# Optimization experiments

Hardware: AMD Instinct MI355X
Metric: run time of the kernel (lower is better)

The kernel has to match this reference:

```python
import jax, jax.numpy as jnp
import numpy as np


def setup_inputs() -> dict:
    key = jax.random.key(0)
    k1, k2 = jax.random.split(key)
    T, H, E = 16384, 4096, 64
    hidden_states = jax.random.normal(k1, (T, H), dtype=jnp.float32)
    W = jax.random.normal(k2, (E, H), dtype=jnp.float32) * 0.02  # init std=0.02
    b = jnp.zeros((E,), dtype=jnp.float32)
    return {"hidden_states": hidden_states, "W": W, "b": b}


def reference(hidden_states, W, b):
    TOPK = 8
    # Linear: [T, H] @ [H, E] + [E] -> [T, E]
    router_logits = jnp.einsum("th,eh->te", hidden_states, W) + b
    router_probs = jax.nn.sigmoid(router_logits)
    routing_weights, routing_indices = jax.lax.top_k(router_probs, TOPK)
    routing_weights = routing_weights / jnp.sum(routing_weights, axis=-1, keepdims=True)
    return routing_weights, routing_indices, router_probs
```

## Files before the change

kernel.cpp:

```cpp
#include <hip/hip_runtime.h>
#include <math.h>

#define H 4096
#define E 64
#define TOPK 8
#define BM 64
#define BK 64
#define NKSTEP (BK / 32)
#define NTILE (H / BK)
#define TAU 1e-4f


typedef __attribute__((ext_vector_type(8))) short bf16x8;
typedef __attribute__((ext_vector_type(4))) float f32x4;

__device__ __forceinline__ unsigned short bf16_rne(float x) {
    unsigned int u = __float_as_uint(x);
    u += 0x7FFFu + ((u >> 16) & 1u);
    return (unsigned short)(u >> 16);
}
__device__ __forceinline__ float bf16_f32(unsigned short h) {
    return __uint_as_float(((unsigned int)h) << 16);
}

#define SPLIT2(F0, F1, HI, LO)                                          \
    {                                                                   \
        const unsigned short h0 = bf16_rne(F0), h1 = bf16_rne(F1);      \
        const unsigned short l0 = bf16_rne((F0) - bf16_f32(h0));        \
        const unsigned short l1 = bf16_rne((F1) - bf16_f32(h1));        \
        HI = (unsigned int)h0 | ((unsigned int)h1 << 16);               \
        LO = (unsigned int)l0 | ((unsigned int)l1 << 16);               \
    }

__global__ __launch_bounds__(256) void w_split(
    const float* __restrict__ W, unsigned short* __restrict__ Whi,
    unsigned short* __restrict__ Wlo)
{
    const size_t t = (size_t)blockIdx.x * 256 + threadIdx.x;
    const float4 v = *(const float4*)(W + t * 4);
    uint2 h, l;
    SPLIT2(v.x, v.y, h.x, l.x);
    SPLIT2(v.z, v.w, h.y, l.y);
    *(uint2*)(Whi + t * 4) = h;
    *(uint2*)(Wlo + t * 4) = l;
}

__global__ __launch_bounds__(512, 2) void router_gemm_topk(
    const float* __restrict__ A, const unsigned short* __restrict__ Whi,
    const unsigned short* __restrict__ Wlo, const float* __restrict__ bias,
    float* __restrict__ weights, float* __restrict__ indices,
    float* __restrict__ probs,
    int* __restrict__ flagcnt, int* __restrict__ flaglist, int cap)
{
    __shared__ unsigned short Ahi[BM][BK];
    __shared__ unsigned short Alo[BM][BK];
    __shared__ unsigned short Bhi[E][BK];
    __shared__ unsigned short Blo[E][BK];
    __shared__ float Llds[BM][E + 1];

    const int tid = threadIdx.x;
    const long row0 = (long)blockIdx.x * BM;

    const int srow = tid >> 3;
    const int sseg = tid & 7;
    const int slot = (sseg ^ (srow & 7)) * 8;

    const float* __restrict__ ap          = A   + (row0 + srow) * H + sseg * 8;
    const unsigned short* __restrict__ wh = Whi + (size_t)srow * H + sseg * 8;
    const unsigned short* __restrict__ wl = Wlo + (size_t)srow * H + sseg * 8;

    const int wv    = tid >> 6;
    const int l     = tid & 63;
    const int rbase = (wv & 3) * 16;
    const int cbase = (wv >> 2) * 32;
    const int lrow  = l & 15;
    const int khalf = l >> 4;

    f32x4 acc0 = {0.f, 0.f, 0.f, 0.f};
    f32x4 acc1 = {0.f, 0.f, 0.f, 0.f};

    float4 pa0 = *(const float4*)(ap + 0);
    float4 pa1 = *(const float4*)(ap + 4);
    uint4  pbh = *(const uint4*)(wh);
    uint4  pbl = *(const uint4*)(wl);

    for (int t = 0; t < NTILE; ++t) {
        uint4 h, lo;
        SPLIT2(pa0.x, pa0.y, h.x, lo.x);
        SPLIT2(pa0.z, pa0.w, h.y, lo.y);
        SPLIT2(pa1.x, pa1.y, h.z, lo.z);
        SPLIT2(pa1.z, pa1.w, h.w, lo.w);
        *(uint4*)(&Ahi[srow][slot]) = h;
        *(uint4*)(&Alo[srow][slot]) = lo;
        *(uint4*)(&Bhi[srow][slot]) = pbh;
        *(uint4*)(&Blo[srow][slot]) = pbl;
        __syncthreads();

        if (t + 1 < NTILE) {
            const int kn = (t + 1) * BK;
            pa0 = *(const float4*)(ap + kn + 0);
            pa1 = *(const float4*)(ap + kn + 4);
            pbh = *(const uint4*)(wh + kn);
            pbl = *(const uint4*)(wl + kn);
        }

#pragma unroll
        for (int s = 0; s < NKSTEP; ++s) {
            const int fs = ((s * 4 + khalf) ^ (lrow & 7)) * 8;
            const bf16x8 fah  = *(const bf16x8*)(&Ahi[rbase + lrow][fs]);
            const bf16x8 fal  = *(const bf16x8*)(&Alo[rbase + lrow][fs]);
            const bf16x8 fbh0 = *(const bf16x8*)(&Bhi[cbase + lrow][fs]);
            const bf16x8 fbl0 = *(const bf16x8*)(&Blo[cbase + lrow][fs]);
            const bf16x8 fbh1 = *(const bf16x8*)(&Bhi[cbase + 16 + lrow][fs]);
            const bf16x8 fbl1 = *(const bf16x8*)(&Blo[cbase + 16 + lrow][fs]);
            acc0 = __builtin_amdgcn_mfma_f32_16x16x32_bf16(fah, fbh0, acc0, 0, 0, 0);
            acc0 = __builtin_amdgcn_mfma_f32_16x16x32_bf16(fah, fbl0, acc0, 0, 0, 0);
            acc0 = __builtin_amdgcn_mfma_f32_16x16x32_bf16(fal, fbh0, acc0, 0, 0, 0);
            acc0 = __builtin_amdgcn_mfma_f32_16x16x32_bf16(fal, fbl0, acc0, 0, 0, 0);
            acc1 = __builtin_amdgcn_mfma_f32_16x16x32_bf16(fah, fbh1, acc1, 0, 0, 0);
            acc1 = __builtin_amdgcn_mfma_f32_16x16x32_bf16(fah, fbl1, acc1, 0, 0, 0);
            acc1 = __builtin_amdgcn_mfma_f32_16x16x32_bf16(fal, fbh1, acc1, 0, 0, 0);
            acc1 = __builtin_amdgcn_mfma_f32_16x16x32_bf16(fal, fbl1, acc1, 0, 0, 0);
        }
        __syncthreads();
    }

    {
        const int c0 = cbase + lrow;
        const int c1 = cbase + 16 + lrow;
        const float b0 = bias[c0], b1 = bias[c1];
#pragma unroll
        for (int r = 0; r < 4; ++r) {
            const int row = rbase + khalf * 4 + r;
            Llds[row][c0] = acc0[r] + b0;
            Llds[row][c1] = acc1[r] + b1;
        }
    }
    __syncthreads();

    {
        const int row = tid >> 3;
        const int c   = (tid & 7) * 8;
        float4 o0, o1;
        o0.x = 1.0f / (1.0f + __expf(-Llds[row][c + 0]));
        o0.y = 1.0f / (1.0f + __expf(-Llds[row][c + 1]));
        o0.z = 1.0f / (1.0f + __expf(-Llds[row][c + 2]));
        o0.w = 1.0f / (1.0f + __expf(-Llds[row][c + 3]));
        o1.x = 1.0f / (1.0f + __expf(-Llds[row][c + 4]));
        o1.y = 1.0f / (1.0f + __expf(-Llds[row][c + 5]));
        o1.z = 1.0f / (1.0f + __expf(-Llds[row][c + 6]));
        o1.w = 1.0f / (1.0f + __expf(-Llds[row][c + 7]));
        *(float4*)(probs + (row0 + row) * E + c + 0) = o0;
        *(float4*)(probs + (row0 + row) * E + c + 4) = o1;
    }

    if (tid < BM) {
        const int r = tid;
        unsigned long long taken = 0ull;
        float sv[TOPK + 1];
        int   si[TOPK + 1];
#pragma unroll
        for (int it = 0; it <= TOPK; ++it) {
            float best = -3.0e38f;
            int   bi   = 0;
            for (int j = 0; j < E; ++j) {
                if (!((taken >> j) & 1ull)) {
                    const float v = Llds[r][j];
                    if (v > best) { best = v; bi = j; }
                }
            }
            taken |= 1ull << bi;
            sv[it] = best;
            si[it] = bi;
        }
        float w8[TOPK];
        float sum = 0.0f;
#pragma unroll
        for (int it = 0; it < TOPK; ++it) {
            w8[it] = 1.0f / (1.0f + __expf(-sv[it]));
            sum += w8[it];
        }
        const float inv = 1.0f / sum;
#pragma unroll
        for (int it = 0; it < TOPK; ++it) {
            weights[(row0 + r) * TOPK + it] = w8[it] * inv;
            indices[(row0 + r) * TOPK + it] = (float)si[it];
        }
        bool amb = false;
#pragma unroll
        for (int it = 0; it < TOPK; ++it) amb |= (sv[it] - sv[it + 1]) < TAU;
        if (amb && cap > 0) {
            const int pos = atomicAdd(flagcnt, 1);
            if (pos < cap) flaglist[pos] = (int)(row0 + r);
        }
    }
}

__global__ __launch_bounds__(256) void router_recheck(
    const float* __restrict__ A, const float* __restrict__ W,
    const float* __restrict__ bias,
    float* __restrict__ weights, float* __restrict__ indices,
    const int* __restrict__ flagcnt, const int* __restrict__ flaglist,
    int cap)
{
    __shared__ double part[4][E];
    __shared__ double lg[E];

    const int e  = threadIdx.x & 63;
    const int kc = threadIdx.x >> 6;

    int n = *flagcnt;
    if (n > cap) n = cap;

    for (int f = blockIdx.x; f < n; f += gridDim.x) {
        const int row = flaglist[f];
        const float* ar = A + (long)row * H + kc * (H / 4);
        const float* wr = W + (long)e   * H + kc * (H / 4);
        double s = 0.0;
        for (int k = 0; k < H / 4; k += 4) {
            const float4 av = *(const float4*)(ar + k);
            const float4 wv = *(const float4*)(wr + k);
            s = fma((double)av.x, (double)wv.x, s);
            s = fma((double)av.y, (double)wv.y, s);
            s = fma((double)av.z, (double)wv.z, s);
            s = fma((double)av.w, (double)wv.w, s);
        }
        part[kc][e] = s;
        __syncthreads();
        if (threadIdx.x < E) {
            const int j = threadIdx.x;
            lg[j] = ((part[0][j] + part[1][j]) + (part[2][j] + part[3][j]))
                    + (double)bias[j];
        }
        __syncthreads();
        if (threadIdx.x == 0) {
            unsigned long long taken = 0ull;
            float wsel[TOPK];
            int   isel[TOPK];
            float psum = 0.0f;
            for (int it = 0; it < TOPK; ++it) {
                double best = -1.0e300;
                int    bi   = 0;
                for (int j = 0; j < E; ++j) {
                    if (!((taken >> j) & 1ull)) {
                        const double v = lg[j];
                        if (v > best) { best = v; bi = j; }
                    }
                }
                taken |= 1ull << bi;
                const float p = 1.0f / (1.0f + __expf(-(float)best));
                wsel[it] = p;
                isel[it] = bi;
                psum += p;
            }
            const float inv = 1.0f / psum;
            for (int it = 0; it < TOPK; ++it) {
                weights[(long)row * TOPK + it] = wsel[it] * inv;
                indices[(long)row * TOPK + it] = (float)isel[it];
            }
        }
        __syncthreads();
    }
}

extern "C" void kernel_launch(void* const* d_in, const int* in_sizes, int n_in,
                              void* d_out, int out_size, void* d_ws, size_t ws_size,
                              hipStream_t stream)
{
    const float* A    = (const float*)d_in[0];
    const float* W    = (const float*)d_in[1];
    const float* bias = (const float*)d_in[2];
    const int T = in_sizes[0] / H;

    float* out     = (float*)d_out;
    float* weights = out;
    float* indices = out + (size_t)T * TOPK;
    float* probs   = out + (size_t)T * 2 * TOPK;

    unsigned short* Whi = (unsigned short*)d_ws;
    unsigned short* Wlo = Whi + (size_t)E * H;
    const size_t W_BYTES = (size_t)E * H * 2 * sizeof(unsigned short);
    int* flagcnt  = (int*)((char*)d_ws + W_BYTES);
    int* flaglist = flagcnt + 4;
    long cap_l = ((long)ws_size - (long)W_BYTES - 16) / 4;
    int  cap   = cap_l < 0 ? 0 : (cap_l > T ? T : (int)cap_l);

    if (cap > 0) hipMemsetAsync(flagcnt, 0, sizeof(int), stream);

    w_split<<<(E * H / 4) / 256, 256, 0, stream>>>(W, Whi, Wlo);
    router_gemm_topk<<<T / BM, 512, 0, stream>>>(A, Whi, Wlo, bias,
                                                 weights, indices, probs,
                                                 flagcnt, flaglist, cap);
    if (cap > 0)
        router_recheck<<<256, 256, 0, stream>>>(A, W, bias, weights, indices,
                                                flagcnt, flaglist, cap);
}
```

Before: 482.1 us.

## Feed MFMA operands directly from global memory with 16-row blocks

Removes the shared-memory staging of A and W tiles and the per-tile barriers. Each wave now loads its MFMA fragments straight from global memory into registers, with two-step register double buffering. Blocks shrink to 16 rows and 128 threads, giving four times as many blocks. The trade-off is that every block re-reads the full bf16 W hi/lo arrays, raising L2 traffic, and A loads become less coalesced per instruction.

```diff
diff --git a/kernel.cpp b/kernel.cpp
--- a/kernel.cpp
+++ b/kernel.cpp
@@ -4,10 +4,7 @@
 #define H 4096
 #define E 64
 #define TOPK 8
-#define BM 64
-#define BK 64
-#define NKSTEP (BK / 32)
-#define NTILE (H / BK)
+#define NK (H / 32)
 #define TAU 1e-4f
 
 
@@ -45,84 +42,82 @@
     *(uint2*)(Wlo + t * 4) = l;
 }
 
-__global__ __launch_bounds__(512, 2) void router_gemm_topk(
+#define KSTEP(A0, A1, BH0, BL0, BH1, BL1, TN)                              \
+    {                                                                      \
+        uint4 h_, lo_;                                                     \
+        SPLIT2((A0).x, (A0).y, h_.x, lo_.x);                               \
+        SPLIT2((A0).z, (A0).w, h_.y, lo_.y);                               \
+        SPLIT2((A1).x, (A1).y, h_.z, lo_.z);                               \
+        SPLIT2((A1).z, (A1).w, h_.w, lo_.w);                               \
+        const bf16x8 fah  = *(const bf16x8*)&h_;                           \
+        const bf16x8 fal  = *(const bf16x8*)&lo_;                          \
+        const uint4 ch0 = BH0, cl0 = BL0, ch1 = BH1, cl1 = BL1;            \
+        if ((TN) < NK) {                                                   \
+            const int kn = (TN) * 32;                                      \
+            A0  = *(const float4*)(ap + kn);                               \
+            A1  = *(const float4*)(ap + kn + 4);                           \
+            BH0 = *(const uint4*)(wh0 + kn);                               \
+            BL0 = *(const uint4*)(wl0 + kn);                               \
+            BH1 = *(const uint4*)(wh1 + kn);                               \
+            BL1 = *(const uint4*)(wl1 + kn);                               \
+        }                                                                  \
+        const bf16x8 fbh0 = *(const bf16x8*)&ch0;                          \
+        const bf16x8 fbl0 = *(const bf16x8*)&cl0;                          \
+        const bf16x8 fbh1 = *(const bf16x8*)&ch1;                          \
+        const bf16x8 fbl1 = *(const bf16x8*)&cl1;                          \
+        acc0 = __builtin_amdgcn_mfma_f32_16x16x32_bf16(fah, fbh0, acc0, 0, 0, 0); \
+        acc0 = __builtin_amdgcn_mfma_f32_16x16x32_bf16(fah, fbl0, acc0, 0, 0, 0); \
+        acc0 = __builtin_amdgcn_mfma_f32_16x16x32_bf16(fal, fbh0, acc0, 0, 0, 0); \
+        acc0 = __builtin_amdgcn_mfma_f32_16x16x32_bf16(fal, fbl0, acc0, 0, 0, 0); \
+        acc1 = __builtin_amdgcn_mfma_f32_16x16x32_bf16(fah, fbh1, acc1, 0, 0, 0); \
+        acc1 = __builtin_amdgcn_mfma_f32_16x16x32_bf16(fah, fbl1, acc1, 0, 0, 0); \
+        acc1 = __builtin_amdgcn_mfma_f32_16x16x32_bf16(fal, fbh1, acc1, 0, 0, 0); \
+        acc1 = __builtin_amdgcn_mfma_f32_16x16x32_bf16(fal, fbl1, acc1, 0, 0, 0); \
+    }
+
+__global__ __launch_bounds__(128, 2) void router_gemm_topk(
     const float* __restrict__ A, const unsigned short* __restrict__ Whi,
     const unsigned short* __restrict__ Wlo, const float* __restrict__ bias,
     float* __restrict__ weights, float* __restrict__ indices,
     float* __restrict__ probs,
     int* __restrict__ flagcnt, int* __restrict__ flaglist, int cap)
 {
-    __shared__ unsigned short Ahi[BM][BK];
-    __shared__ unsigned short Alo[BM][BK];
-    __shared__ unsigned short Bhi[E][BK];
-    __shared__ unsigned short Blo[E][BK];
-    __shared__ float Llds[BM][E + 1];
-
-    const int tid = threadIdx.x;
-    const long row0 = (long)blockIdx.x * BM;
-
-    const int srow = tid >> 3;
-    const int sseg = tid & 7;
-    const int slot = (sseg ^ (srow & 7)) * 8;
-
-    const float* __restrict__ ap          = A   + (row0 + srow) * H + sseg * 8;
-    const unsigned short* __restrict__ wh = Whi + (size_t)srow * H + sseg * 8;
-    const unsigned short* __restrict__ wl = Wlo + (size_t)srow * H + sseg * 8;
-
+    __shared__ float Llds[16][E + 1];
+
+    const int tid   = threadIdx.x;
     const int wv    = tid >> 6;
     const int l     = tid & 63;
-    const int rbase = (wv & 3) * 16;
-    const int cbase = (wv >> 2) * 32;
     const int lrow  = l & 15;
     const int khalf = l >> 4;
+    const int cbase = wv * 32;
+    const long row0 = (long)blockIdx.x * 16;
+
+    const float* __restrict__ ap =
+        A + (row0 + lrow) * H + khalf * 8;
+    const unsigned short* __restrict__ wh0 = Whi + (size_t)(cbase + lrow) * H + khalf * 8;
+    const unsigned short* __restrict__ wl0 = Wlo + (size_t)(cbase + lrow) * H + khalf * 8;
+    const unsigned short* __restrict__ wh1 = Whi + (size_t)(cbase + 16 + lrow) * H + khalf * 8;
+    const unsigned short* __restrict__ wl1 = Wlo + (size_t)(cbase + 16 + lrow) * H + khalf * 8;
 
     f32x4 acc0 = {0.f, 0.f, 0.f, 0.f};
     f32x4 acc1 = {0.f, 0.f, 0.f, 0.f};
 
-    float4 pa0 = *(const float4*)(ap + 0);
-    float4 pa1 = *(const float4*)(ap + 4);
-    uint4  pbh = *(const uint4*)(wh);
-    uint4  pbl = *(const uint4*)(wl);
-
-    for (int t = 0; t < NTILE; ++t) {
-        uint4 h, lo;
-        SPLIT2(pa0.x, pa0.y, h.x, lo.x);
-        SPLIT2(pa0.z, pa0.w, h.y, lo.y);
-        SPLIT2(pa1.x, pa1.y, h.z, lo.z);
-        SPLIT2(pa1.z, pa1.w, h.w, lo.w);
-        *(uint4*)(&Ahi[srow][slot]) = h;
-        *(uint4*)(&Alo[srow][slot]) = lo;
-        *(uint4*)(&Bhi[srow][slot]) = pbh;
-        *(uint4*)(&Blo[srow][slot]) = pbl;
-        __syncthreads();
-
-        if (t + 1 < NTILE) {
-            const int kn = (t + 1) * BK;
-            pa0 = *(const float4*)(ap + kn + 0);
-            pa1 = *(const float4*)(ap + kn + 4);
-            pbh = *(const uint4*)(wh + kn);
-            pbl = *(const uint4*)(wl + kn);
-        }
-
-#pragma unroll
-        for (int s = 0; s < NKSTEP; ++s) {
-            const int fs = ((s * 4 + khalf) ^ (lrow & 7)) * 8;
-            const bf16x8 fah  = *(const bf16x8*)(&Ahi[rbase + lrow][fs]);
-            const bf16x8 fal  = *(const bf16x8*)(&Alo[rbase + lrow][fs]);
-            const bf16x8 fbh0 = *(const bf16x8*)(&Bhi[cbase + lrow][fs]);
-            const bf16x8 fbl0 = *(const bf16x8*)(&Blo[cbase + lrow][fs]);
-            const bf16x8 fbh1 = *(const bf16x8*)(&Bhi[cbase + 16 + lrow][fs]);
-            const bf16x8 fbl1 = *(const bf16x8*)(&Blo[cbase + 16 + lrow][fs]);
-            acc0 = __builtin_amdgcn_mfma_f32_16x16x32_bf16(fah, fbh0, acc0, 0, 0, 0);
-            acc0 = __builtin_amdgcn_mfma_f32_16x16x32_bf16(fah, fbl0, acc0, 0, 0, 0);
-            acc0 = __builtin_amdgcn_mfma_f32_16x16x32_bf16(fal, fbh0, acc0, 0, 0, 0);
-            acc0 = __builtin_amdgcn_mfma_f32_16x16x32_bf16(fal, fbl0, acc0, 0, 0, 0);
-            acc1 = __builtin_amdgcn_mfma_f32_16x16x32_bf16(fah, fbh1, acc1, 0, 0, 0);
-            acc1 = __builtin_amdgcn_mfma_f32_16x16x32_bf16(fah, fbl1, acc1, 0, 0, 0);
-            acc1 = __builtin_amdgcn_mfma_f32_16x16x32_bf16(fal, fbh1, acc1, 0, 0, 0);
-            acc1 = __builtin_amdgcn_mfma_f32_16x16x32_bf16(fal, fbl1, acc1, 0, 0, 0);
-        }
-        __syncthreads();
+    float4 a0X = *(const float4*)(ap + 0);
+    float4 a1X = *(const float4*)(ap + 4);
+    uint4  h0X = *(const uint4*)(wh0);
+    uint4  l0X = *(const uint4*)(wl0);
+    uint4  h1X = *(const uint4*)(wh1);
+    uint4  l1X = *(const uint4*)(wl1);
+    float4 a0Y = *(const float4*)(ap + 32);
+    float4 a1Y = *(const float4*)(ap + 36);
+    uint4  h0Y = *(const uint4*)(wh0 + 32);
+    uint4  l0Y = *(const uint4*)(wl0 + 32);
+    uint4  h1Y = *(const uint4*)(wh1 + 32);
+    uint4  l1Y = *(const uint4*)(wl1 + 32);
+
+    for (int t = 0; t < NK; t += 2) {
+        KSTEP(a0X, a1X, h0X, l0X, h1X, l1X, t + 2)
+        KSTEP(a0Y, a1Y, h0Y, l0Y, h1Y, l1Y, t + 3)
     }
 
     {
@@ -131,7 +126,7 @@
         const float b0 = bias[c0], b1 = bias[c1];
 #pragma unroll
         for (int r = 0; r < 4; ++r) {
-            const int row = rbase + khalf * 4 + r;
+            const int row = khalf * 4 + r;
             Llds[row][c0] = acc0[r] + b0;
             Llds[row][c1] = acc1[r] + b1;
         }
@@ -154,7 +149,7 @@
         *(float4*)(probs + (row0 + row) * E + c + 4) = o1;
     }
 
-    if (tid < BM) {
+    if (tid < 16) {
         const int r = tid;
         unsigned long long taken = 0ull;
         float sv[TOPK + 1];
@@ -288,7 +283,7 @@
     if (cap > 0) hipMemsetAsync(flagcnt, 0, sizeof(int), stream);
 
     w_split<<<(E * H / 4) / 256, 256, 0, stream>>>(W, Whi, Wlo);
-    router_gemm_topk<<<T / BM, 512, 0, stream>>>(A, Whi, Wlo, bias,
+    router_gemm_topk<<<T / 16, 128, 0, stream>>>(A, Whi, Wlo, bias,
                                                  weights, indices, probs,
                                                  flagcnt, flaglist, cap);
     if (cap > 0)
```

Result: slower. 556.3 us (+15.4%).

## Shrink row tile to 16 and use 256-thread blocks for more CTAs

Applied to the files above, without the earlier changes.

Reduces the per-block row tile from 64 to 16 and the block size from 512 to 256 threads. Each wave now computes one 16x16 output tile over 16 of the 64 experts, and W tile loading is redistributed across all threads. This quadruples the grid so more blocks can be resident per CU and hide global-load latency. In exchange, each block re-reads the full split W from cache, so W traffic per row of A increases fourfold.

```diff
diff --git a/kernel.cpp b/kernel.cpp
--- a/kernel.cpp
+++ b/kernel.cpp
@@ -4,9 +4,8 @@
 #define H 4096
 #define E 64
 #define TOPK 8
-#define BM 64
+#define BM 16
 #define BK 64
-#define NKSTEP (BK / 32)
 #define NTILE (H / BK)
 #define TAU 1e-4f
 
@@ -45,7 +44,7 @@
     *(uint2*)(Wlo + t * 4) = l;
 }
 
-__global__ __launch_bounds__(512, 2) void router_gemm_topk(
+__global__ __launch_bounds__(256, 4) void router_gemm_topk(
     const float* __restrict__ A, const unsigned short* __restrict__ Whi,
     const unsigned short* __restrict__ Wlo, const float* __restrict__ bias,
     float* __restrict__ weights, float* __restrict__ indices,
@@ -61,97 +60,96 @@
     const int tid = threadIdx.x;
     const long row0 = (long)blockIdx.x * BM;
 
-    const int srow = tid >> 3;
-    const int sseg = tid & 7;
-    const int slot = (sseg ^ (srow & 7)) * 8;
-
-    const float* __restrict__ ap          = A   + (row0 + srow) * H + sseg * 8;
-    const unsigned short* __restrict__ wh = Whi + (size_t)srow * H + sseg * 8;
-    const unsigned short* __restrict__ wl = Wlo + (size_t)srow * H + sseg * 8;
+    const int arow  = tid >> 3;
+    const int aseg  = tid & 7;
+    const int aslot = (aseg ^ (arow & 7)) * 8;
+    const int wrow  = tid >> 2;
+    const int wseg  = (tid & 3) * 2;
+    const int wslot0 = ((wseg + 0) ^ (wrow & 7)) * 8;
+    const int wslot1 = ((wseg + 1) ^ (wrow & 7)) * 8;
+
+    const float* __restrict__ ap          = A   + (row0 + arow) * H + aseg * 8;
+    const unsigned short* __restrict__ wh = Whi + (size_t)wrow * H + wseg * 8;
+    const unsigned short* __restrict__ wl = Wlo + (size_t)wrow * H + wseg * 8;
 
     const int wv    = tid >> 6;
     const int l     = tid & 63;
-    const int rbase = (wv & 3) * 16;
-    const int cbase = (wv >> 2) * 32;
     const int lrow  = l & 15;
     const int khalf = l >> 4;
 
-    f32x4 acc0 = {0.f, 0.f, 0.f, 0.f};
-    f32x4 acc1 = {0.f, 0.f, 0.f, 0.f};
-
-    float4 pa0 = *(const float4*)(ap + 0);
-    float4 pa1 = *(const float4*)(ap + 4);
-    uint4  pbh = *(const uint4*)(wh);
-    uint4  pbl = *(const uint4*)(wl);
+    f32x4 acc = {0.f, 0.f, 0.f, 0.f};
+
+    float4 pa0, pa1;
+    if (tid < 128) {
+        pa0 = *(const float4*)(ap + 0);
+        pa1 = *(const float4*)(ap + 4);
+    }
+    uint4 pwh0 = *(const uint4*)(wh + 0);
+    uint4 pwh1 = *(const uint4*)(wh + 8);
+    uint4 pwl0 = *(const uint4*)(wl + 0);
+    uint4 pwl1 = *(const uint4*)(wl + 8);
 
     for (int t = 0; t < NTILE; ++t) {
-        uint4 h, lo;
-        SPLIT2(pa0.x, pa0.y, h.x, lo.x);
-        SPLIT2(pa0.z, pa0.w, h.y, lo.y);
-        SPLIT2(pa1.x, pa1.y, h.z, lo.z);
-        SPLIT2(pa1.z, pa1.w, h.w, lo.w);
-        *(uint4*)(&Ahi[srow][slot]) = h;
-        *(uint4*)(&Alo[srow][slot]) = lo;
-        *(uint4*)(&Bhi[srow][slot]) = pbh;
-        *(uint4*)(&Blo[srow][slot]) = pbl;
+        if (tid < 128) {
+            uint4 h, lo;
+            SPLIT2(pa0.x, pa0.y, h.x, lo.x);
+            SPLIT2(pa0.z, pa0.w, h.y, lo.y);
+            SPLIT2(pa1.x, pa1.y, h.z, lo.z);
+            SPLIT2(pa1.z, pa1.w, h.w, lo.w);
+            *(uint4*)(&Ahi[arow][aslot]) = h;
+            *(uint4*)(&Alo[arow][aslot]) = lo;
+        }
+        *(uint4*)(&Bhi[wrow][wslot0]) = pwh0;
+        *(uint4*)(&Bhi[wrow][wslot1]) = pwh1;
+        *(uint4*)(&Blo[wrow][wslot0]) = pwl0;
+        *(uint4*)(&Blo[wrow][wslot1]) = pwl1;
         __syncthreads();
 
         if (t + 1 < NTILE) {
             const int kn = (t + 1) * BK;
-            pa0 = *(const float4*)(ap + kn + 0);
-            pa1 = *(const float4*)(ap + kn + 4);
-            pbh = *(const uint4*)(wh + kn);
-            pbl = *(const uint4*)(wl + kn);
-        }
-
-#pragma unroll
-        for (int s = 0; s < NKSTEP; ++s) {
+            if (tid < 128) {
+                pa0 = *(const float4*)(ap + kn + 0);
+                pa1 = *(const float4*)(ap + kn + 4);
+            }
+            pwh0 = *(const uint4*)(wh + kn + 0);
+            pwh1 = *(const uint4*)(wh + kn + 8);
+            pwl0 = *(const uint4*)(wl + kn + 0);
+            pwl1 = *(const uint4*)(wl + kn + 8);
+        }
+
+#pragma unroll
+        for (int s = 0; s < BK / 32; ++s) {
             const int fs = ((s * 4 + khalf) ^ (lrow & 7)) * 8;
-            const bf16x8 fah  = *(const bf16x8*)(&Ahi[rbase + lrow][fs]);
-            const bf16x8 fal  = *(const bf16x8*)(&Alo[rbase + lrow][fs]);
-            const bf16x8 fbh0 = *(const bf16x8*)(&Bhi[cbase + lrow][fs]);
-            const bf16x8 fbl0 = *(const bf16x8*)(&Blo[cbase + lrow][fs]);
-            const bf16x8 fbh1 = *(const bf16x8*)(&Bhi[cbase + 16 + lrow][fs]);
-            const bf16x8 fbl1 = *(const bf16x8*)(&Blo[cbase + 16 + lrow][fs]);
-            acc0 = __builtin_amdgcn_mfma_f32_16x16x32_bf16(fah, fbh0, acc0, 0, 0, 0);
-            acc0 = __builtin_amdgcn_mfma_f32_16x16x32_bf16(fah, fbl0, acc0, 0, 0, 0);
-            acc0 = __builtin_amdgcn_mfma_f32_16x16x32_bf16(fal, fbh0, acc0, 0, 0, 0);
-            acc0 = __builtin_amdgcn_mfma_f32_16x16x32_bf16(fal, fbl0, acc0, 0, 0, 0);
-            acc1 = __builtin_amdgcn_mfma_f32_16x16x32_bf16(fah, fbh1, acc1, 0, 0, 0);
-            acc1 = __builtin_amdgcn_mfma_f32_16x16x32_bf16(fah, fbl1, acc1, 0, 0, 0);
-            acc1 = __builtin_amdgcn_mfma_f32_16x16x32_bf16(fal, fbh1, acc1, 0, 0, 0);
-            acc1 = __builtin_amdgcn_mfma_f32_16x16x32_bf16(fal, fbl1, acc1, 0, 0, 0);
+            const bf16x8 fah = *(const bf16x8*)(&Ahi[lrow][fs]);
+            const bf16x8 fal = *(const bf16x8*)(&Alo[lrow][fs]);
+            const bf16x8 fbh = *(const bf16x8*)(&Bhi[wv * 16 + lrow][fs]);
+            const bf16x8 fbl = *(const bf16x8*)(&Blo[wv * 16 + lrow][fs]);
+            acc = __builtin_amdgcn_mfma_f32_16x16x32_bf16(fah, fbh, acc, 0, 0, 0);
+            acc = __builtin_amdgcn_mfma_f32_16x16x32_bf16(fah, fbl, acc, 0, 0, 0);
+            acc = __builtin_amdgcn_mfma_f32_16x16x32_bf16(fal, fbh, acc, 0, 0, 0);
+            acc = __builtin_amdgcn_mfma_f32_16x16x32_bf16(fal, fbl, acc, 0, 0, 0);
         }
         __syncthreads();
     }
 
     {
-        const int c0 = cbase + lrow;
-        const int c1 = cbase + 16 + lrow;
-        const float b0 = bias[c0], b1 = bias[c1];
-#pragma unroll
-        for (int r = 0; r < 4; ++r) {
-            const int row = rbase + khalf * 4 + r;
-            Llds[row][c0] = acc0[r] + b0;
-            Llds[row][c1] = acc1[r] + b1;
-        }
+        const int c = wv * 16 + lrow;
+        const float b = bias[c];
+#pragma unroll
+        for (int r = 0; r < 4; ++r)
+            Llds[khalf * 4 + r][c] = acc[r] + b;
     }
     __syncthreads();
 
     {
-        const int row = tid >> 3;
-        const int c   = (tid & 7) * 8;
-        float4 o0, o1;
-        o0.x = 1.0f / (1.0f + __expf(-Llds[row][c + 0]));
-        o0.y = 1.0f / (1.0f + __expf(-Llds[row][c + 1]));
-        o0.z = 1.0f / (1.0f + __expf(-Llds[row][c + 2]));
-        o0.w = 1.0f / (1.0f + __expf(-Llds[row][c + 3]));
-        o1.x = 1.0f / (1.0f + __expf(-Llds[row][c + 4]));
-        o1.y = 1.0f / (1.0f + __expf(-Llds[row][c + 5]));
-        o1.z = 1.0f / (1.0f + __expf(-Llds[row][c + 6]));
-        o1.w = 1.0f / (1.0f + __expf(-Llds[row][c + 7]));
-        *(float4*)(probs + (row0 + row) * E + c + 0) = o0;
-        *(float4*)(probs + (row0 + row) * E + c + 4) = o1;
+        const int row = tid >> 4;
+        const int c   = (tid & 15) * 4;
+        float4 o;
+        o.x = 1.0f / (1.0f + __expf(-Llds[row][c + 0]));
+        o.y = 1.0f / (1.0f + __expf(-Llds[row][c + 1]));
+        o.z = 1.0f / (1.0f + __expf(-Llds[row][c + 2]));
+        o.w = 1.0f / (1.0f + __expf(-Llds[row][c + 3]));
+        *(float4*)(probs + (row0 + row) * E + c) = o;
     }
 
     if (tid < BM) {
@@ -288,7 +286,7 @@
     if (cap > 0) hipMemsetAsync(flagcnt, 0, sizeof(int), stream);
 
     w_split<<<(E * H / 4) / 256, 256, 0, stream>>>(W, Whi, Wlo);
-    router_gemm_topk<<<T / BM, 512, 0, stream>>>(A, Whi, Wlo, bias,
+    router_gemm_topk<<<T / BM, 256, 0, stream>>>(A, Whi, Wlo, bias,
                                                  weights, indices, probs,
                                                  flagcnt, flaglist, cap);
     if (cap > 0)
```

Measured after the change: 489.2 us. Within noise of the previous version (+1.5%).
